# Performance work log

Measured on AMD Instinct MI355X. Metric: run time of the kernel, lower is better.

## Reference

```python
import jax, jax.numpy as jnp
import numpy as np

NQ = 4
B = 524288
# CNOT wiring from ansatz: control=(NQ-2-i)%NQ, target=(NQ-1-i)%NQ -> [(2,3),(1,2),(0,1),(3,0)]
CNOT_PAIRS = [((NQ - 2 - i) % NQ, (NQ - 1 - i) % NQ) for i in range(NQ)]


def _c64(a):
    return a.astype(jnp.complex64)


def rx_gate(a):
    # PennyLane RX(a) = [[cos(a/2), -i sin(a/2)], [-i sin(a/2), cos(a/2)]]
    c = _c64(jnp.cos(a / 2)); s = _c64(jnp.sin(a / 2))
    return jnp.stack([jnp.stack([c, -1j * s], -1), jnp.stack([-1j * s, c], -1)], -2)


def ry_gate(a):
    c = _c64(jnp.cos(a / 2)); s = _c64(jnp.sin(a / 2))
    return jnp.stack([jnp.stack([c, -s], -1), jnp.stack([s, c], -1)], -2)


def rz_gate(a):
    e = jnp.exp(-1j * _c64(a) / 2)
    z = jnp.zeros_like(e)
    return jnp.stack([jnp.stack([e, z], -1), jnp.stack([z, jnp.conj(e)], -1)], -2)


def apply_1q(state, gate, wire):
    # state: [B,2,2,2,2]; gate: [2,2] (shared) or [B,2,2] (per-sample)
    s = jnp.moveaxis(state, wire + 1, -1)
    if gate.ndim == 2:
        s = jnp.einsum('ij,...j->...i', gate, s)
    else:
        s = jnp.einsum('bij,b...j->b...i', gate, s)
    return jnp.moveaxis(s, -1, wire + 1)


def apply_cnot(state, c, t):
    s = jnp.moveaxis(state, (c + 1, t + 1), (-2, -1))  # [..., control, target]
    s = jnp.stack([s[..., 0, :], s[..., 1, ::-1]], axis=-2)  # flip target where control=1
    return jnp.moveaxis(s, (-2, -1), (c + 1, t + 1))


def circuit(weights, x):
    b = x.shape[0]
    state = jnp.zeros((b,) + (2,) * NQ, jnp.complex64)
    state = state.at[(slice(None),) + (0,) * NQ].set(1.0)  # |0000>
    for layer in range(4):
        p = weights[8 * layer: 8 * (layer + 1)]
        # embedding: RX(x_i) on wire i (per-sample angles)
        for i in range(NQ):
            state = apply_1q(state, rx_gate(x[:, i]), i)
        # ansatz: RY then RZ (shared weight angles), then cyclic CNOTs
        for i in range(NQ):
            state = apply_1q(state, ry_gate(p[i]), i)
        for i in range(NQ):
            state = apply_1q(state, rz_gate(p[i + NQ]), i)
        for c_, t_ in CNOT_PAIRS:
            state = apply_cnot(state, c_, t_)
    probs = jnp.abs(state) ** 2  # [B,2,2,2,2] real
    outs = []
    for i in range(NQ):
        axes = tuple(a for a in range(1, NQ + 1) if a != i + 1)
        m = probs.sum(axes)  # [B,2]
        outs.append(m[:, 0] - m[:, 1])  # <Z_i> = P(0) - P(1)
    return jnp.stack(outs, -1).astype(jnp.float32)


def setup_inputs() -> dict:
    key = jax.random.key(0)
    kx, kw = jax.random.split(key)
    x = jax.random.normal(kx, (B, NQ), dtype=jnp.float32)
    weights = 0.1 * jax.random.normal(kw, (8 * NQ,), dtype=jnp.float32)
    return {"x": x, "weights": weights}


def reference(x, weights):
    return circuit(weights, x)
```

## Files before the change

### kernel.cpp

```cpp
#include <hip/hip_runtime.h>


#define GATE_APPLY(K0, K1) do {                                         \
    float a0r = r##K0, a0i = i##K0, a1r = r##K1, a1i = i##K1;           \
    r##K0 = gr * a0r - gi * a0i + dr * a1r - di * a1i;                  \
    i##K0 = gr * a0i + gi * a0r + dr * a1i + di * a1r;                  \
    r##K1 = gr * a1r + gi * a1i - dr * a0r - di * a0i;                  \
    i##K1 = gr * a1i - gi * a1r - dr * a0i + di * a0r;                  \
  } while (0)

#define SU2_W0 do { GATE_APPLY(0,8); GATE_APPLY(1,9); GATE_APPLY(2,10); GATE_APPLY(3,11); \
                    GATE_APPLY(4,12); GATE_APPLY(5,13); GATE_APPLY(6,14); GATE_APPLY(7,15); } while (0)
#define SU2_W1 do { GATE_APPLY(0,4); GATE_APPLY(1,5); GATE_APPLY(2,6); GATE_APPLY(3,7);   \
                    GATE_APPLY(8,12); GATE_APPLY(9,13); GATE_APPLY(10,14); GATE_APPLY(11,15); } while (0)
#define SU2_W2 do { GATE_APPLY(0,2); GATE_APPLY(1,3); GATE_APPLY(4,6); GATE_APPLY(5,7);   \
                    GATE_APPLY(8,10); GATE_APPLY(9,11); GATE_APPLY(12,14); GATE_APPLY(13,15); } while (0)
#define SU2_W3 do { GATE_APPLY(0,1); GATE_APPLY(2,3); GATE_APPLY(4,5); GATE_APPLY(6,7);   \
                    GATE_APPLY(8,9); GATE_APPLY(10,11); GATE_APPLY(12,13); GATE_APPLY(14,15); } while (0)

#define SWAPK(A, B) do { float t_r = r##A; r##A = r##B; r##B = t_r;     \
                         float t_i = i##A; i##A = i##B; i##B = t_i; } while (0)
#define CNOT_23 do { SWAPK(2,3);  SWAPK(6,7);  SWAPK(10,11); SWAPK(14,15); } while (0)
#define CNOT_12 do { SWAPK(4,6);  SWAPK(5,7);  SWAPK(12,14); SWAPK(13,15); } while (0)
#define CNOT_01 do { SWAPK(8,12); SWAPK(9,13); SWAPK(10,14); SWAPK(11,15); } while (0)
#define CNOT_30 do { SWAPK(1,9);  SWAPK(3,11); SWAPK(5,13); SWAPK(7,15); } while (0)

#define L0_EXPAND(K, KP) do {                                           \
    float e_ar = r##K, e_ai = i##K;                                     \
    r##KP = -(dr * e_ar) - di * e_ai;                                   \
    i##KP = di * e_ar - dr * e_ai;                                      \
    r##K  = gr * e_ar - gi * e_ai;                                      \
    i##K  = gr * e_ai + gi * e_ar;                                      \
  } while (0)

__device__ __forceinline__ void make_g2(const float4* Msh, int idx,
                                        float c, float s,
                                        float& gr, float& gi, float& dr, float& di) {
  float4 m = Msh[idx];
  gr = m.x * c + m.w * s;
  gi = m.y * c - m.z * s;
  dr = m.y * s + m.z * c;
  di = m.w * c - m.x * s;
}

__device__ __forceinline__ void make_g2_real(const float4* Msh, int idx,
                                             float c, float s,
                                             float& gr, float& gi, float& dr, float& di) {
  float4 m = Msh[idx];
  gr = m.x * c;
  gi = -(m.z * s);
  dr = m.z * c;
  di = -(m.x * s);
}

__global__ __launch_bounds__(256) void qlayer_main(const float* __restrict__ x,
                                                   const float* __restrict__ w,
                                                   float* __restrict__ out) {
  __shared__ float4 Msh[16];
  int tid = threadIdx.x;
  if (tid < 16) {
    int l = tid >> 2, q = tid & 3;
    float ay = 0.5f * w[8 * l + q];
    float az = (l == 3) ? 0.0f : 0.5f * w[8 * l + 4 + q];
    float cy = __cosf(ay), sy = __sinf(ay);
    float cz = __cosf(az), sz = __sinf(az);
    Msh[tid] = make_float4(cz * cy, -sz * cy, -cz * sy, sz * sy);
  }

  int t = blockIdx.x * blockDim.x + tid;
  float4 xv = reinterpret_cast<const float4*>(x)[t];
  float cx0 = __cosf(0.5f * xv.x), sx0 = __sinf(0.5f * xv.x);
  float cx1 = __cosf(0.5f * xv.y), sx1 = __sinf(0.5f * xv.y);
  float cx2 = __cosf(0.5f * xv.z), sx2 = __sinf(0.5f * xv.z);
  float cx3 = __cosf(0.5f * xv.w), sx3 = __sinf(0.5f * xv.w);

  __syncthreads();

  float r0, r1, r2, r3, r4, r5, r6, r7, r8, r9, r10, r11, r12, r13, r14, r15;
  float i0, i1, i2, i3, i4, i5, i6, i7, i8, i9, i10, i11, i12, i13, i14, i15;

  float gr, gi, dr, di;

  make_g2(Msh, 3, cx3, sx3, gr, gi, dr, di);
  r0 = gr;  i0 = gi;
  r1 = -dr; i1 = di;
  make_g2(Msh, 2, cx2, sx2, gr, gi, dr, di);
  L0_EXPAND(1, 3); L0_EXPAND(0, 2);
  make_g2(Msh, 1, cx1, sx1, gr, gi, dr, di);
  L0_EXPAND(3, 7); L0_EXPAND(2, 6); L0_EXPAND(1, 5); L0_EXPAND(0, 4);
  make_g2(Msh, 0, cx0, sx0, gr, gi, dr, di);
  L0_EXPAND(7, 15); L0_EXPAND(6, 14); L0_EXPAND(5, 13); L0_EXPAND(4, 12);
  L0_EXPAND(3, 11); L0_EXPAND(2, 10); L0_EXPAND(1, 9);  L0_EXPAND(0, 8);
  CNOT_23; CNOT_12; CNOT_01; CNOT_30;

#pragma unroll
  for (int l = 1; l < 3; ++l) {
    make_g2(Msh, l * 4 + 0, cx0, sx0, gr, gi, dr, di); SU2_W0;
    make_g2(Msh, l * 4 + 1, cx1, sx1, gr, gi, dr, di); SU2_W1;
    make_g2(Msh, l * 4 + 2, cx2, sx2, gr, gi, dr, di); SU2_W2;
    make_g2(Msh, l * 4 + 3, cx3, sx3, gr, gi, dr, di); SU2_W3;
    CNOT_23; CNOT_12; CNOT_01; CNOT_30;
  }

  make_g2_real(Msh, 12, cx0, sx0, gr, gi, dr, di); SU2_W0;
  make_g2_real(Msh, 13, cx1, sx1, gr, gi, dr, di); SU2_W1;
  make_g2_real(Msh, 14, cx2, sx2, gr, gi, dr, di); SU2_W2;
  make_g2_real(Msh, 15, cx3, sx3, gr, gi, dr, di); SU2_W3;
  CNOT_23; CNOT_12; CNOT_01; CNOT_30;

  float p0  = r0  * r0  + i0  * i0,  p1  = r1  * r1  + i1  * i1;
  float p2  = r2  * r2  + i2  * i2,  p3  = r3  * r3  + i3  * i3;
  float p4  = r4  * r4  + i4  * i4,  p5  = r5  * r5  + i5  * i5;
  float p6  = r6  * r6  + i6  * i6,  p7  = r7  * r7  + i7  * i7;
  float p8  = r8  * r8  + i8  * i8,  p9  = r9  * r9  + i9  * i9;
  float p10 = r10 * r10 + i10 * i10, p11 = r11 * r11 + i11 * i11;
  float p12 = r12 * r12 + i12 * i12, p13 = r13 * r13 + i13 * i13;
  float p14 = r14 * r14 + i14 * i14, p15 = r15 * r15 + i15 * i15;

  float s20 = p0 + p1,   d20 = p0 - p1;
  float s21 = p2 + p3,   d21 = p2 - p3;
  float s22 = p4 + p5,   d22 = p4 - p5;
  float s23 = p6 + p7,   d23 = p6 - p7;
  float s24 = p8 + p9,   d24 = p8 - p9;
  float s25 = p10 + p11, d25 = p10 - p11;
  float s26 = p12 + p13, d26 = p12 - p13;
  float s27 = p14 + p15, d27 = p14 - p15;
  float o3 = ((d20 + d21) + (d22 + d23)) + ((d24 + d25) + (d26 + d27));

  float s40 = s20 + s21, d40 = s20 - s21;
  float s41 = s22 + s23, d41 = s22 - s23;
  float s42 = s24 + s25, d42 = s24 - s25;
  float s43 = s26 + s27, d43 = s26 - s27;
  float o2 = (d40 + d41) + (d42 + d43);

  float s8a = s40 + s41, s8b = s42 + s43;
  float d8a = s40 - s41, d8b = s42 - s43;
  float o1 = d8a + d8b;
  float o0 = s8a - s8b;

  reinterpret_cast<float4*>(out)[t] = make_float4(o0, o1, o2, o3);
}

extern "C" void kernel_launch(void* const* d_in, const int* in_sizes, int n_in,
                              void* d_out, int out_size, void* d_ws, size_t ws_size,
                              hipStream_t stream) {
  const float* x = (const float*)d_in[0];
  const float* w = (const float*)d_in[1];
  float* out = (float*)d_out;
  int nb = in_sizes[0] / 4;

  int blocks = nb / 256;
  hipLaunchKernelGGL(qlayer_main, dim3(blocks), dim3(256), 0, stream, x, w, out);
}
```

Measured before the change: 90.29 us.

## Process four samples per thread using packed float2 math

```diff
diff --git a/kernel.cpp b/kernel.cpp
--- a/kernel.cpp
+++ b/kernel.cpp
@@ -1,62 +1,87 @@
 #include <hip/hip_runtime.h>
 
 
-#define GATE_APPLY(K0, K1) do {                                         \
-    float a0r = r##K0, a0i = i##K0, a1r = r##K1, a1i = i##K1;           \
-    r##K0 = gr * a0r - gi * a0i + dr * a1r - di * a1i;                  \
-    i##K0 = gr * a0i + gi * a0r + dr * a1i + di * a1r;                  \
-    r##K1 = gr * a1r + gi * a1i - dr * a0r - di * a0i;                  \
-    i##K1 = gr * a1i - gi * a1r - dr * a0i + di * a0r;                  \
+typedef float v2f __attribute__((ext_vector_type(2)));
+
+#define GATE_APPLY(S, K0, K1) do {                                        \
+    v2f a0r = sr##S##_##K0, a0i = si##S##_##K0;                           \
+    v2f a1r = sr##S##_##K1, a1i = si##S##_##K1;                           \
+    sr##S##_##K0 = gr##S * a0r - gi##S * a0i + dr##S * a1r - di##S * a1i; \
+    si##S##_##K0 = gr##S * a0i + gi##S * a0r + dr##S * a1i + di##S * a1r; \
+    sr##S##_##K1 = gr##S * a1r + gi##S * a1i - dr##S * a0r - di##S * a0i; \
+    si##S##_##K1 = gr##S * a1i - gi##S * a1r - dr##S * a0i + di##S * a0r; \
   } while (0)
 
-#define SU2_W0 do { GATE_APPLY(0,8); GATE_APPLY(1,9); GATE_APPLY(2,10); GATE_APPLY(3,11); \
-                    GATE_APPLY(4,12); GATE_APPLY(5,13); GATE_APPLY(6,14); GATE_APPLY(7,15); } while (0)
-#define SU2_W1 do { GATE_APPLY(0,4); GATE_APPLY(1,5); GATE_APPLY(2,6); GATE_APPLY(3,7);   \
-                    GATE_APPLY(8,12); GATE_APPLY(9,13); GATE_APPLY(10,14); GATE_APPLY(11,15); } while (0)
-#define SU2_W2 do { GATE_APPLY(0,2); GATE_APPLY(1,3); GATE_APPLY(4,6); GATE_APPLY(5,7);   \
-                    GATE_APPLY(8,10); GATE_APPLY(9,11); GATE_APPLY(12,14); GATE_APPLY(13,15); } while (0)
-#define SU2_W3 do { GATE_APPLY(0,1); GATE_APPLY(2,3); GATE_APPLY(4,5); GATE_APPLY(6,7);   \
-                    GATE_APPLY(8,9); GATE_APPLY(10,11); GATE_APPLY(12,13); GATE_APPLY(14,15); } while (0)
+#define SU2_W0(S) do { GATE_APPLY(S,0,8);  GATE_APPLY(S,1,9);   GATE_APPLY(S,2,10);  GATE_APPLY(S,3,11); \
+                       GATE_APPLY(S,4,12); GATE_APPLY(S,5,13);  GATE_APPLY(S,6,14);  GATE_APPLY(S,7,15); } while (0)
+#define SU2_W1(S) do { GATE_APPLY(S,0,4);  GATE_APPLY(S,1,5);   GATE_APPLY(S,2,6);   GATE_APPLY(S,3,7);  \
+                       GATE_APPLY(S,8,12); GATE_APPLY(S,9,13);  GATE_APPLY(S,10,14); GATE_APPLY(S,11,15); } while (0)
+#define SU2_W2(S) do { GATE_APPLY(S,0,2);  GATE_APPLY(S,1,3);   GATE_APPLY(S,4,6);   GATE_APPLY(S,5,7);  \
+                       GATE_APPLY(S,8,10); GATE_APPLY(S,9,11);  GATE_APPLY(S,12,14); GATE_APPLY(S,13,15); } while (0)
+#define SU2_W3(S) do { GATE_APPLY(S,0,1);  GATE_APPLY(S,2,3);   GATE_APPLY(S,4,5);   GATE_APPLY(S,6,7);  \
+                       GATE_APPLY(S,8,9);  GATE_APPLY(S,10,11); GATE_APPLY(S,12,13); GATE_APPLY(S,14,15); } while (0)
 
-#define SWAPK(A, B) do { float t_r = r##A; r##A = r##B; r##B = t_r;     \
-                         float t_i = i##A; i##A = i##B; i##B = t_i; } while (0)
-#define CNOT_23 do { SWAPK(2,3);  SWAPK(6,7);  SWAPK(10,11); SWAPK(14,15); } while (0)
-#define CNOT_12 do { SWAPK(4,6);  SWAPK(5,7);  SWAPK(12,14); SWAPK(13,15); } while (0)
-#define CNOT_01 do { SWAPK(8,12); SWAPK(9,13); SWAPK(10,14); SWAPK(11,15); } while (0)
-#define CNOT_30 do { SWAPK(1,9);  SWAPK(3,11); SWAPK(5,13); SWAPK(7,15); } while (0)
+#define SWAPK(S, A, B) do { v2f t_r = sr##S##_##A; sr##S##_##A = sr##S##_##B; sr##S##_##B = t_r; \
+                            v2f t_i = si##S##_##A; si##S##_##A = si##S##_##B; si##S##_##B = t_i; } while (0)
+#define CNOTS(S) do { SWAPK(S,2,3);  SWAPK(S,6,7);  SWAPK(S,10,11); SWAPK(S,14,15); \
+                      SWAPK(S,4,6);  SWAPK(S,5,7);  SWAPK(S,12,14); SWAPK(S,13,15); \
+                      SWAPK(S,8,12); SWAPK(S,9,13); SWAPK(S,10,14); SWAPK(S,11,15); \
+                      SWAPK(S,1,9);  SWAPK(S,3,11); SWAPK(S,5,13); SWAPK(S,7,15); } while (0)
 
-#define L0_EXPAND(K, KP) do {                                           \
-    float e_ar = r##K, e_ai = i##K;                                     \
-    r##KP = -(dr * e_ar) - di * e_ai;                                   \
-    i##KP = di * e_ar - dr * e_ai;                                      \
-    r##K  = gr * e_ar - gi * e_ai;                                      \
-    i##K  = gr * e_ai + gi * e_ar;                                      \
+#define L0_EXPAND(S, K, KP) do {                          \
+    v2f e_ar = sr##S##_##K, e_ai = si##S##_##K;           \
+    sr##S##_##KP = -(dr##S * e_ar) - di##S * e_ai;        \
+    si##S##_##KP = di##S * e_ar - dr##S * e_ai;           \
+    sr##S##_##K  = gr##S * e_ar - gi##S * e_ai;           \
+    si##S##_##K  = gr##S * e_ai + gi##S * e_ar;           \
   } while (0)
 
-__device__ __forceinline__ void make_g2(const float4* Msh, int idx,
-                                        float c, float s,
-                                        float& gr, float& gi, float& dr, float& di) {
-  float4 m = Msh[idx];
-  gr = m.x * c + m.w * s;
-  gi = m.y * c - m.z * s;
-  dr = m.y * s + m.z * c;
-  di = m.w * c - m.x * s;
-}
+#define MAKE_G2_AB(IDX, Q) do {                                           \
+    v2f m_ar = Msh[(IDX) * 4 + 0], m_ai = Msh[(IDX) * 4 + 1];             \
+    v2f m_br = Msh[(IDX) * 4 + 2], m_bi = Msh[(IDX) * 4 + 3];             \
+    grA = m_ar * cxA##Q + m_bi * sxA##Q;                                  \
+    giA = m_ai * cxA##Q - m_br * sxA##Q;                                  \
+    drA = m_ai * sxA##Q + m_br * cxA##Q;                                  \
+    diA = m_bi * cxA##Q - m_ar * sxA##Q;                                  \
+    grB = m_ar * cxB##Q + m_bi * sxB##Q;                                  \
+    giB = m_ai * cxB##Q - m_br * sxB##Q;                                  \
+    drB = m_ai * sxB##Q + m_br * cxB##Q;                                  \
+    diB = m_bi * cxB##Q - m_ar * sxB##Q;                                  \
+  } while (0)
 
-__device__ __forceinline__ void make_g2_real(const float4* Msh, int idx,
-                                             float c, float s,
-                                             float& gr, float& gi, float& dr, float& di) {
-  float4 m = Msh[idx];
-  gr = m.x * c;
-  gi = -(m.z * s);
-  dr = m.z * c;
-  di = -(m.x * s);
-}
+#define MAKE_G2_REAL_AB(IDX, Q) do {                                      \
+    v2f m_ar = Msh[(IDX) * 4 + 0], m_br = Msh[(IDX) * 4 + 2];             \
+    grA = m_ar * cxA##Q;  giA = -(m_br * sxA##Q);                         \
+    drA = m_br * cxA##Q;  diA = -(m_ar * sxA##Q);                         \
+    grB = m_ar * cxB##Q;  giB = -(m_br * sxB##Q);                         \
+    drB = m_br * cxB##Q;  diB = -(m_ar * sxB##Q);                         \
+  } while (0)
+
+#define PSQ(S, K) (sr##S##_##K * sr##S##_##K + si##S##_##K * si##S##_##K)
+
+#define MEASURE(S) do {                                                   \
+    v2f p0 = PSQ(S,0),  p1 = PSQ(S,1),  p2 = PSQ(S,2),  p3 = PSQ(S,3);    \
+    v2f p4 = PSQ(S,4),  p5 = PSQ(S,5),  p6 = PSQ(S,6),  p7 = PSQ(S,7);    \
+    v2f p8 = PSQ(S,8),  p9 = PSQ(S,9),  pa = PSQ(S,10), pb = PSQ(S,11);   \
+    v2f pc = PSQ(S,12), pd = PSQ(S,13), pe = PSQ(S,14), pf = PSQ(S,15);   \
+    v2f s20 = p0 + p1, d20 = p0 - p1,  s21 = p2 + p3, d21 = p2 - p3;      \
+    v2f s22 = p4 + p5, d22 = p4 - p5,  s23 = p6 + p7, d23 = p6 - p7;      \
+    v2f s24 = p8 + p9, d24 = p8 - p9,  s25 = pa + pb, d25 = pa - pb;      \
+    v2f s26 = pc + pd, d26 = pc - pd,  s27 = pe + pf, d27 = pe - pf;      \
+    o3##S = ((d20 + d21) + (d22 + d23)) + ((d24 + d25) + (d26 + d27));    \
+    v2f s40 = s20 + s21, d40 = s20 - s21, s41 = s22 + s23, d41 = s22 - s23; \
+    v2f s42 = s24 + s25, d42 = s24 - s25, s43 = s26 + s27, d43 = s26 - s27; \
+    o2##S = (d40 + d41) + (d42 + d43);                                    \
+    v2f s8a = s40 + s41, s8b = s42 + s43;                                 \
+    v2f d8a = s40 - s41, d8b = s42 - s43;                                 \
+    o1##S = d8a + d8b;                                                    \
+    o0##S = s8a - s8b;                                                    \
+  } while (0)
 
 __global__ __launch_bounds__(256) void qlayer_main(const float* __restrict__ x,
                                                    const float* __restrict__ w,
                                                    float* __restrict__ out) {
-  __shared__ float4 Msh[16];
+  __shared__ v2f Msh[16 * 4];
   int tid = threadIdx.x;
   if (tid < 16) {
     int l = tid >> 2, q = tid & 3;
@@ -64,81 +89,87 @@
     float az = (l == 3) ? 0.0f : 0.5f * w[8 * l + 4 + q];
     float cy = __cosf(ay), sy = __sinf(ay);
     float cz = __cosf(az), sz = __sinf(az);
-    Msh[tid] = make_float4(cz * cy, -sz * cy, -cz * sy, sz * sy);
+    float ar = cz * cy, ai = -sz * cy, br = -cz * sy, bi = sz * sy;
+    Msh[tid * 4 + 0] = v2f{ar, ar};
+    Msh[tid * 4 + 1] = v2f{ai, ai};
+    Msh[tid * 4 + 2] = v2f{br, br};
+    Msh[tid * 4 + 3] = v2f{bi, bi};
   }
 
   int t = blockIdx.x * blockDim.x + tid;
-  float4 xv = reinterpret_cast<const float4*>(x)[t];
-  float cx0 = __cosf(0.5f * xv.x), sx0 = __sinf(0.5f * xv.x);
-  float cx1 = __cosf(0.5f * xv.y), sx1 = __sinf(0.5f * xv.y);
-  float cx2 = __cosf(0.5f * xv.z), sx2 = __sinf(0.5f * xv.z);
-  float cx3 = __cosf(0.5f * xv.w), sx3 = __sinf(0.5f * xv.w);
+  const float4* x4 = reinterpret_cast<const float4*>(x);
+  float4 xv0 = x4[4 * t + 0], xv1 = x4[4 * t + 1];
+  float4 xv2 = x4[4 * t + 2], xv3 = x4[4 * t + 3];
+
+  v2f cxA0 = v2f{__cosf(0.5f * xv0.x), __cosf(0.5f * xv1.x)};
+  v2f sxA0 = v2f{__sinf(0.5f * xv0.x), __sinf(0.5f * xv1.x)};
+  v2f cxA1 = v2f{__cosf(0.5f * xv0.y), __cosf(0.5f * xv1.y)};
+  v2f sxA1 = v2f{__sinf(0.5f * xv0.y), __sinf(0.5f * xv1.y)};
+  v2f cxA2 = v2f{__cosf(0.5f * xv0.z), __cosf(0.5f * xv1.z)};
+  v2f sxA2 = v2f{__sinf(0.5f * xv0.z), __sinf(0.5f * xv1.z)};
+  v2f cxA3 = v2f{__cosf(0.5f * xv0.w), __cosf(0.5f * xv1.w)};
+  v2f sxA3 = v2f{__sinf(0.5f * xv0.w), __sinf(0.5f * xv1.w)};
+  v2f cxB0 = v2f{__cosf(0.5f * xv2.x), __cosf(0.5f * xv3.x)};
+  v2f sxB0 = v2f{__sinf(0.5f * xv2.x), __sinf(0.5f * xv3.x)};
+  v2f cxB1 = v2f{__cosf(0.5f * xv2.y), __cosf(0.5f * xv3.y)};
+  v2f sxB1 = v2f{__sinf(0.5f * xv2.y), __sinf(0.5f * xv3.y)};
+  v2f cxB2 = v2f{__cosf(0.5f * xv2.z), __cosf(0.5f * xv3.z)};
+  v2f sxB2 = v2f{__sinf(0.5f * xv2.z), __sinf(0.5f * xv3.z)};
+  v2f cxB3 = v2f{__cosf(0.5f * xv2.w), __cosf(0.5f * xv3.w)};
+  v2f sxB3 = v2f{__sinf(0.5f * xv2.w), __sinf(0.5f * xv3.w)};
 
   __syncthreads();
 
-  float r0, r1, r2, r3, r4, r5, r6, r7, r8, r9, r10, r11, r12, r13, r14, r15;
-  float i0, i1, i2, i3, i4, i5, i6, i7, i8, i9, i10, i11, i12, i13, i14, i15;
+  v2f srA_0, srA_1, srA_2, srA_3, srA_4, srA_5, srA_6, srA_7;
+  v2f srA_8, srA_9, srA_10, srA_11, srA_12, srA_13, srA_14, srA_15;
+  v2f siA_0, siA_1, siA_2, siA_3, siA_4, siA_5, siA_6, siA_7;
+  v2f siA_8, siA_9, siA_10, siA_11, siA_12, siA_13, siA_14, siA_15;
+  v2f srB_0, srB_1, srB_2, srB_3, srB_4, srB_5, srB_6, srB_7;
+  v2f srB_8, srB_9, srB_10, srB_11, srB_12, srB_13, srB_14, srB_15;
+  v2f siB_0, siB_1, siB_2, siB_3, siB_4, siB_5, siB_6, siB_7;
+  v2f siB_8, siB_9, siB_10, siB_11, siB_12, siB_13, siB_14, siB_15;
+  v2f grA, giA, drA, diA, grB, giB, drB, diB;
 
-  float gr, gi, dr, di;
-
-  make_g2(Msh, 3, cx3, sx3, gr, gi, dr, di);
-  r0 = gr;  i0 = gi;
-  r1 = -dr; i1 = di;
-  make_g2(Msh, 2, cx2, sx2, gr, gi, dr, di);
-  L0_EXPAND(1, 3); L0_EXPAND(0, 2);
-  make_g2(Msh, 1, cx1, sx1, gr, gi, dr, di);
-  L0_EXPAND(3, 7); L0_EXPAND(2, 6); L0_EXPAND(1, 5); L0_EXPAND(0, 4);
-  make_g2(Msh, 0, cx0, sx0, gr, gi, dr, di);
-  L0_EXPAND(7, 15); L0_EXPAND(6, 14); L0_EXPAND(5, 13); L0_EXPAND(4, 12);
-  L0_EXPAND(3, 11); L0_EXPAND(2, 10); L0_EXPAND(1, 9);  L0_EXPAND(0, 8);
-  CNOT_23; CNOT_12; CNOT_01; CNOT_30;
+  MAKE_G2_AB(3, 3);
+  srA_0 = grA;  siA_0 = giA;  srA_1 = -drA; siA_1 = diA;
+  srB_0 = grB;  siB_0 = giB;  srB_1 = -drB; siB_1 = diB;
+  MAKE_G2_AB(2, 2);
+  L0_EXPAND(A, 1, 3); L0_EXPAND(A, 0, 2);
+  L0_EXPAND(B, 1, 3); L0_EXPAND(B, 0, 2);
+  MAKE_G2_AB(1, 1);
+  L0_EXPAND(A, 3, 7); L0_EXPAND(A, 2, 6); L0_EXPAND(A, 1, 5); L0_EXPAND(A, 0, 4);
+  L0_EXPAND(B, 3, 7); L0_EXPAND(B, 2, 6); L0_EXPAND(B, 1, 5); L0_EXPAND(B, 0, 4);
+  MAKE_G2_AB(0, 0);
+  L0_EXPAND(A, 7, 15); L0_EXPAND(A, 6, 14); L0_EXPAND(A, 5, 13); L0_EXPAND(A, 4, 12);
+  L0_EXPAND(A, 3, 11); L0_EXPAND(A, 2, 10); L0_EXPAND(A, 1, 9);  L0_EXPAND(A, 0, 8);
+  L0_EXPAND(B, 7, 15); L0_EXPAND(B, 6, 14); L0_EXPAND(B, 5, 13); L0_EXPAND(B, 4, 12);
+  L0_EXPAND(B, 3, 11); L0_EXPAND(B, 2, 10); L0_EXPAND(B, 1, 9);  L0_EXPAND(B, 0, 8);
+  CNOTS(A); CNOTS(B);
 
 #pragma unroll
   for (int l = 1; l < 3; ++l) {
-    make_g2(Msh, l * 4 + 0, cx0, sx0, gr, gi, dr, di); SU2_W0;
-    make_g2(Msh, l * 4 + 1, cx1, sx1, gr, gi, dr, di); SU2_W1;
-    make_g2(Msh, l * 4 + 2, cx2, sx2, gr, gi, dr, di); SU2_W2;
-    make_g2(Msh, l * 4 + 3, cx3, sx3, gr, gi, dr, di); SU2_W3;
-    CNOT_23; CNOT_12; CNOT_01; CNOT_30;
+    MAKE_G2_AB(l * 4 + 0, 0); SU2_W0(A); SU2_W0(B);
+    MAKE_G2_AB(l * 4 + 1, 1); SU2_W1(A); SU2_W1(B);
+    MAKE_G2_AB(l * 4 + 2, 2); SU2_W2(A); SU2_W2(B);
+    MAKE_G2_AB(l * 4 + 3, 3); SU2_W3(A); SU2_W3(B);
+    CNOTS(A); CNOTS(B);
   }
 
-  make_g2_real(Msh, 12, cx0, sx0, gr, gi, dr, di); SU2_W0;
-  make_g2_real(Msh, 13, cx1, sx1, gr, gi, dr, di); SU2_W1;
-  make_g2_real(Msh, 14, cx2, sx2, gr, gi, dr, di); SU2_W2;
-  make_g2_real(Msh, 15, cx3, sx3, gr, gi, dr, di); SU2_W3;
-  CNOT_23; CNOT_12; CNOT_01; CNOT_30;
+  MAKE_G2_REAL_AB(12, 0); SU2_W0(A); SU2_W0(B);
+  MAKE_G2_REAL_AB(13, 1); SU2_W1(A); SU2_W1(B);
+  MAKE_G2_REAL_AB(14, 2); SU2_W2(A); SU2_W2(B);
+  MAKE_G2_REAL_AB(15, 3); SU2_W3(A); SU2_W3(B);
+  CNOTS(A); CNOTS(B);
 
-  float p0  = r0  * r0  + i0  * i0,  p1  = r1  * r1  + i1  * i1;
-  float p2  = r2  * r2  + i2  * i2,  p3  = r3  * r3  + i3  * i3;
-  float p4  = r4  * r4  + i4  * i4,  p5  = r5  * r5  + i5  * i5;
-  float p6  = r6  * r6  + i6  * i6,  p7  = r7  * r7  + i7  * i7;
-  float p8  = r8  * r8  + i8  * i8,  p9  = r9  * r9  + i9  * i9;
-  float p10 = r10 * r10 + i10 * i10, p11 = r11 * r11 + i11 * i11;
-  float p12 = r12 * r12 + i12 * i12, p13 = r13 * r13 + i13 * i13;
-  float p14 = r14 * r14 + i14 * i14, p15 = r15 * r15 + i15 * i15;
+  v2f o0A, o1A, o2A, o3A, o0B, o1B, o2B, o3B;
+  MEASURE(A);
+  MEASURE(B);
 
-  float s20 = p0 + p1,   d20 = p0 - p1;
-  float s21 = p2 + p3,   d21 = p2 - p3;
-  float s22 = p4 + p5,   d22 = p4 - p5;
-  float s23 = p6 + p7,   d23 = p6 - p7;
-  float s24 = p8 + p9,   d24 = p8 - p9;
-  float s25 = p10 + p11, d25 = p10 - p11;
-  float s26 = p12 + p13, d26 = p12 - p13;
-  float s27 = p14 + p15, d27 = p14 - p15;
-  float o3 = ((d20 + d21) + (d22 + d23)) + ((d24 + d25) + (d26 + d27));
-
-  float s40 = s20 + s21, d40 = s20 - s21;
-  float s41 = s22 + s23, d41 = s22 - s23;
-  float s42 = s24 + s25, d42 = s24 - s25;
-  float s43 = s26 + s27, d43 = s26 - s27;
-  float o2 = (d40 + d41) + (d42 + d43);
-
-  float s8a = s40 + s41, s8b = s42 + s43;
-  float d8a = s40 - s41, d8b = s42 - s43;
-  float o1 = d8a + d8b;
-  float o0 = s8a - s8b;
-
-  reinterpret_cast<float4*>(out)[t] = make_float4(o0, o1, o2, o3);
+  float4* o4 = reinterpret_cast<float4*>(out);
+  o4[4 * t + 0] = make_float4(o0A.x, o1A.x, o2A.x, o3A.x);
+  o4[4 * t + 1] = make_float4(o0A.y, o1A.y, o2A.y, o3A.y);
+  o4[4 * t + 2] = make_float4(o0B.x, o1B.x, o2B.x, o3B.x);
+  o4[4 * t + 3] = make_float4(o0B.y, o1B.y, o2B.y, o3B.y);
 }
 
 extern "C" void kernel_launch(void* const* d_in, const int* in_sizes, int n_in,
@@ -148,7 +179,7 @@
   const float* w = (const float*)d_in[1];
   float* out = (float*)d_out;
   int nb = in_sizes[0] / 4;
-
-  int blocks = nb / 256;
+  int threads = nb / 4;
+  int blocks = threads / 256;
   hipLaunchKernelGGL(qlayer_main, dim3(blocks), dim3(256), 0, stream, x, w, out);
 }
```

After: 78.17 us. 1.16x faster.
